# Performance work log

Measured on AMD Instinct MI355X. Metric: run time of the kernel, lower is better.

The kernel has to match this reference:

```python
import jax, jax.numpy as jnp
import numpy as np

# Module config (matches init_kwargs)
T, B, C = 2048, 8, 1024   # seq_len, batch, input_size
H, K = 16, 31             # num_heads, kernel_size
PAD_L = 30                # padding_l (causal)


def setup_inputs() -> dict:
    key = jax.random.key(0)
    k1, k2 = jax.random.split(key)
    x = jax.random.normal(k1, (T, B, C), dtype=jnp.float32)
    # nn.Parameter(num_heads, kernel_size), xavier-init approximated by randn
    weight = jax.random.normal(k2, (H, K), dtype=jnp.float32)
    return {"x": x, "weight": weight}


def reference(x, weight):
    # x: (T, B, C); weight: (H, K)
    # weight_softmax=True: softmax over kernel taps per head
    w = jax.nn.softmax(weight, axis=-1)  # (H, K)
    # permute to (B, C, T) as the CUDA kernel expects
    x_bct = jnp.transpose(x, (1, 2, 0))
    # expand per-head kernel to per-channel depthwise kernel: (C, 1, K)
    w_ck = jnp.repeat(w, C // H, axis=0)[:, None, :]
    # lightconv: out[b,c,t] = sum_k w[head(c),k] * x_pad[b,c,t+k],
    # left pad = PAD_L, right pad = K-1-PAD_L (causal when PAD_L=K-1).
    # conv_general_dilated is cross-correlation, matching the CUDA kernel.
    out = jax.lax.conv_general_dilated(
        x_bct, w_ck,
        window_strides=(1,),
        padding=[(PAD_L, K - 1 - PAD_L)],
        dimension_numbers=("NCH", "OIH", "NCH"),
        feature_group_count=C,
    )  # (B, C, T)
    # bias=False, so just permute back to (T, B, C)
    return jnp.transpose(out, (2, 0, 1))
```

## Files before the change

kernel.cpp:

```cpp
#include <hip/hip_runtime.h>
#include <math.h>

#define T_LEN 2048
#define B_SZ  8
#define C_SZ  1024
#define NH    16
#define KW    31
#define HALO  (KW - 1)
#define TT    16
#define CHUNK 128
#define NTILE (CHUNK / TT)
#define RING  64
#define WIN   (TT + HALO)
#define ROWSTRIDE (B_SZ * C_SZ)

#define GLOBAL_AS(p) ((const __attribute__((address_space(1))) void*)(p))
#define LDS_AS(p)    ((__attribute__((address_space(3))) void*)(p))

__global__ __launch_bounds__(64, 2) void lightconv_kernel(
    const float* __restrict__ x, const float* __restrict__ weight,
    float* __restrict__ out) {
  __shared__ float ring[RING][64];
  const int lane = threadIdx.x;

  const int cgrp = blockIdx.x & 15;
  const int tc   = blockIdx.x >> 4;
  const int b    = blockIdx.y;
  const int c0   = cgrp * 64;
  const int tb   = tc * CHUNK;

  float wv[KW];
  float m = -1e30f;
#pragma unroll
  for (int k = 0; k < KW; ++k) {
    wv[k] = weight[cgrp * KW + k];
    m = fmaxf(m, wv[k]);
  }
  float s = 0.f;
#pragma unroll
  for (int k = 0; k < KW; ++k) {
    wv[k] = expf(wv[k] - m);
    s += wv[k];
  }
  const float inv = 1.f / s;
  float wk[KW];
#pragma unroll
  for (int k = 0; k < KW; ++k) {
    wk[k] = __uint_as_float(
        __builtin_amdgcn_readfirstlane(__float_as_uint(wv[k] * inv)));
  }

  const float* xbase = x + (size_t)b * C_SZ + c0;

  if (tb == 0) {
#pragma unroll
    for (int i = 0; i < HALO; ++i) {
      ring[(2048 - HALO + i) & (RING - 1)][lane] = 0.f;
    }
#pragma unroll
    for (int i = 0; i < TT; ++i) {
      const float* gp = xbase + (size_t)i * ROWSTRIDE + lane;
      __builtin_amdgcn_global_load_lds(GLOBAL_AS(gp),
                                       LDS_AS(&ring[i & (RING - 1)][0]), 4, 0, 0);
    }
  } else {
#pragma unroll
    for (int i = 0; i < WIN; ++i) {
      const int t = tb - HALO + i;
      const float* gp = xbase + (size_t)t * ROWSTRIDE + lane;
      __builtin_amdgcn_global_load_lds(GLOBAL_AS(gp),
                                       LDS_AS(&ring[(t + 2048) & (RING - 1)][0]),
                                       4, 0, 0);
    }
  }

#pragma unroll 1
  for (int j = 0; j < NTILE; ++j) {
    const int tstart = tb + j * TT;

    if (j + 1 < NTILE) {
#pragma unroll
      for (int r = 0; r < TT; ++r) {
        const int t = tstart + TT + r;
        const float* gp = xbase + (size_t)t * ROWSTRIDE + lane;
        __builtin_amdgcn_global_load_lds(GLOBAL_AS(gp),
                                         LDS_AS(&ring[(t + 2048) & (RING - 1)][0]),
                                         4, 0, 0);
      }
    }
    if (j == 0 || j == NTILE - 1) {
      asm volatile("s_waitcnt vmcnt(16)" ::: "memory");
    } else {
      asm volatile("s_waitcnt vmcnt(31)" ::: "memory");
    }
    __builtin_amdgcn_sched_barrier(0);

    float xv[WIN];
#pragma unroll
    for (int i = 0; i < WIN; ++i) {
      const int t = tstart - HALO + i;
      xv[i] = ring[(t + 2048) & (RING - 1)][lane];
    }
    float* op = out + ((size_t)tstart * B_SZ + b) * C_SZ + c0 + lane;
#pragma unroll
    for (int o = 0; o < TT; ++o) {
      float a = 0.f;
#pragma unroll
      for (int k = 0; k < KW; ++k) a = fmaf(wk[k], xv[o + k], a);
      op[(size_t)o * ROWSTRIDE] = a;
    }
  }
}

extern "C" void kernel_launch(void* const* d_in, const int* in_sizes, int n_in,
                              void* d_out, int out_size, void* d_ws, size_t ws_size,
                              hipStream_t stream) {
  const float* x = (const float*)d_in[0];
  const float* w = (const float*)d_in[1];
  float* out = (float*)d_out;
  (void)in_sizes; (void)n_in; (void)out_size; (void)d_ws; (void)ws_size;

  dim3 grid((C_SZ / 64) * (T_LEN / CHUNK), B_SZ);
  dim3 block(64);
  lightconv_kernel<<<grid, block, 0, stream>>>(x, w, out);
}
```

Baseline: 33.48 us.

## Use 16-byte global-to-LDS loads with two-tile-deep prefetch and halved time tile

Switches the global-to-LDS copies from 4-byte-per-lane to 16-byte-per-lane transfers, so each instruction brings in four time rows at once. The tile length drops from 16 to 8 and prefetch runs two tiles ahead, with the tile loop unrolled by eight so ring indices become compile-time constants. The aim is fewer load instructions and deeper latency hiding. In exchange the vmcnt wait counts are hand-tuned and fragile, and the layout of the 16-byte LDS writes must line up with the ring rows.

```diff
diff --git a/kernel.cpp b/kernel.cpp
--- a/kernel.cpp
+++ b/kernel.cpp
@@ -7,7 +7,7 @@
 #define NH    16
 #define KW    31
 #define HALO  (KW - 1)
-#define TT    16
+#define TT    8
 #define CHUNK 128
 #define NTILE (CHUNK / TT)
 #define RING  64
@@ -51,63 +51,70 @@
   }
 
   const float* xbase = x + (size_t)b * C_SZ + c0;
+  const int lane_off = (lane >> 4) * ROWSTRIDE + (lane & 15) * 4;
 
   if (tb == 0) {
 #pragma unroll
-    for (int i = 0; i < HALO; ++i) {
-      ring[(2048 - HALO + i) & (RING - 1)][lane] = 0.f;
-    }
+    for (int i = 0; i < 32; ++i) ring[32 + i][lane] = 0.f;
 #pragma unroll
-    for (int i = 0; i < TT; ++i) {
-      const float* gp = xbase + (size_t)i * ROWSTRIDE + lane;
+    for (int r4 = 0; r4 < 2; ++r4) {
+      const float* gp = xbase + (size_t)(r4 * 4) * ROWSTRIDE + lane_off;
       __builtin_amdgcn_global_load_lds(GLOBAL_AS(gp),
-                                       LDS_AS(&ring[i & (RING - 1)][0]), 4, 0, 0);
+                                       LDS_AS(&ring[r4 * 4][0]), 16, 0, 0);
     }
   } else {
 #pragma unroll
-    for (int i = 0; i < WIN; ++i) {
-      const int t = tb - HALO + i;
-      const float* gp = xbase + (size_t)t * ROWSTRIDE + lane;
+    for (int r4 = 0; r4 < 10; ++r4) {
+      const float* gp = xbase + (size_t)(tb - 32 + r4 * 4) * ROWSTRIDE + lane_off;
       __builtin_amdgcn_global_load_lds(GLOBAL_AS(gp),
-                                       LDS_AS(&ring[(t + 2048) & (RING - 1)][0]),
-                                       4, 0, 0);
+                                       LDS_AS(&ring[(32 + 4 * r4) & (RING - 1)][0]),
+                                       16, 0, 0);
     }
+  }
+#pragma unroll
+  for (int r4 = 0; r4 < 2; ++r4) {
+    const float* gp = xbase + (size_t)(tb + TT + r4 * 4) * ROWSTRIDE + lane_off;
+    __builtin_amdgcn_global_load_lds(GLOBAL_AS(gp),
+                                     LDS_AS(&ring[8 + r4 * 4][0]), 16, 0, 0);
   }
 
 #pragma unroll 1
-  for (int j = 0; j < NTILE; ++j) {
-    const int tstart = tb + j * TT;
+  for (int jo = 0; jo < 2; ++jo) {
+#pragma unroll
+    for (int jj = 0; jj < NTILE / 2; ++jj) {
+      const int j = jo * 8 + jj;
+      const int tstart = tb + jo * 64 + jj * TT;
 
-    if (j + 1 < NTILE) {
+      if (j <= NTILE - 3) {
 #pragma unroll
-      for (int r = 0; r < TT; ++r) {
-        const int t = tstart + TT + r;
-        const float* gp = xbase + (size_t)t * ROWSTRIDE + lane;
-        __builtin_amdgcn_global_load_lds(GLOBAL_AS(gp),
-                                         LDS_AS(&ring[(t + 2048) & (RING - 1)][0]),
-                                         4, 0, 0);
+        for (int r4 = 0; r4 < 2; ++r4) {
+          const float* gp =
+              xbase + (size_t)(tstart + 2 * TT + r4 * 4) * ROWSTRIDE + lane_off;
+          __builtin_amdgcn_global_load_lds(
+              GLOBAL_AS(gp),
+              LDS_AS(&ring[(8 * jj + 16 + r4 * 4) & (RING - 1)][0]), 16, 0, 0);
+        }
       }
-    }
-    if (j == 0 || j == NTILE - 1) {
-      asm volatile("s_waitcnt vmcnt(16)" ::: "memory");
-    } else {
-      asm volatile("s_waitcnt vmcnt(31)" ::: "memory");
-    }
-    __builtin_amdgcn_sched_barrier(0);
+      if (j == 0)                asm volatile("s_waitcnt vmcnt(4)"  ::: "memory");
+      else if (j == 1)           asm volatile("s_waitcnt vmcnt(12)" ::: "memory");
+      else if (j == NTILE - 2)   asm volatile("s_waitcnt vmcnt(18)" ::: "memory");
+      else if (j == NTILE - 1)   asm volatile("s_waitcnt vmcnt(16)" ::: "memory");
+      else                       asm volatile("s_waitcnt vmcnt(20)" ::: "memory");
+      __builtin_amdgcn_sched_barrier(0);
 
-    float xv[WIN];
+      float xv[WIN];
 #pragma unroll
-    for (int i = 0; i < WIN; ++i) {
-      const int t = tstart - HALO + i;
-      xv[i] = ring[(t + 2048) & (RING - 1)][lane];
-    }
-    float* op = out + ((size_t)tstart * B_SZ + b) * C_SZ + c0 + lane;
+      for (int i = 0; i < WIN; ++i) {
+        xv[i] = ring[(8 * jj + i + 34) & (RING - 1)][lane];
+      }
+      float* op = out + ((size_t)tstart * B_SZ + b) * C_SZ + c0 + lane;
 #pragma unroll
-    for (int o = 0; o < TT; ++o) {
-      float a = 0.f;
+      for (int o = 0; o < TT; ++o) {
+        float a = 0.f;
 #pragma unroll
-      for (int k = 0; k < KW; ++k) a = fmaf(wk[k], xv[o + k], a);
-      op[(size_t)o * ROWSTRIDE] = a;
+        for (int k = 0; k < KW; ++k) a = fmaf(wk[k], xv[o + k], a);
+        op[(size_t)o * ROWSTRIDE] = a;
+      }
     }
   }
 }
```

Measured after the change: 30.80 us. 8.0% less time.
